# Optimization experiments

Hardware: AMD Instinct MI355X
Metric: run time of the kernel (lower is better)

The kernel has to match this reference:

```python
import jax, jax.numpy as jnp
import numpy as np

BLKQ = 64
BLKK = 64
TOPK_RATIO = 0.2


def setup_inputs() -> dict:
    key = jax.random.key(0)
    ks = jax.random.split(key, 5)
    B, H, L, D = 1, 16, 2048, 64
    q = jax.random.normal(ks[0], (B, H, L, D), dtype=jnp.float32)
    k = jax.random.normal(ks[1], (B, H, L, D), dtype=jnp.float32)
    v = jax.random.normal(ks[2], (B, H, L, D), dtype=jnp.float32)
    # proj_l params (zero-init in source; random here so the branch is exercised)
    W_proj = jax.random.normal(ks[3], (D, D), dtype=jnp.float32) * 0.02
    b_proj = jax.random.normal(ks[4], (D,), dtype=jnp.float32) * 0.02
    return {"q": q, "k": k, "v": v, "W_proj": W_proj, "b_proj": b_proj}


def _block_lut(q, k, topk_ratio, blkq, blkk):
    # q,k: [B,H,L,D]. Mean-pool blocks, score, take top-k key blocks per query block.
    B, H, L, D = q.shape
    M, N = L // blkq, L // blkk
    q_blocks = q.reshape(B, H, M, blkq, D).mean(axis=3)   # [B,H,M,D]
    k_blocks = k.reshape(B, H, N, blkk, D).mean(axis=3)   # [B,H,N,D]
    block_scores = jnp.einsum("bhmd,bhnd->bhmn", q_blocks, k_blocks)
    topk = min(N, max(1, int(topk_ratio * N)))
    _, lut = jax.lax.top_k(block_scores, topk)            # [B,H,M,topk] int32
    return lut, topk, M, N


def reference(q, k, v, W_proj, b_proj):
    B, H, L, D = q.shape
    lut, topk, M, N = _block_lut(q, k, TOPK_RATIO, BLKQ, BLKK)

    # ---- block-sparse softmax attention ----
    block_mask = jnp.any(jax.nn.one_hot(lut, N, dtype=jnp.bool_), axis=3)  # [B,H,M,N]
    mask = jnp.repeat(jnp.repeat(block_mask, BLKQ, axis=2), BLKK, axis=3)  # [B,H,L,L]
    scale = 1.0 / jnp.sqrt(jnp.asarray(D, q.dtype))
    scores = jnp.einsum("bhld,bhkd->bhlk", q, k) * scale
    scores = jnp.where(mask, scores, -jnp.inf)
    attn = jax.nn.softmax(scores, axis=-1)  # every row has >= topk*BLKK valid keys
    o_s = jnp.einsum("bhlk,bhkd->bhld", attn, v)

    # ---- linear attention (softmax feature map over D) ----
    q_feat = jax.nn.softmax(q, axis=-1)
    k_feat = jax.nn.softmax(k, axis=-1)
    kv_sum = jnp.einsum("bhld,bhle->bhde", k_feat, v)      # [B,H,D,D]
    k_sum = k_feat.sum(axis=2)                              # [B,H,D]
    num = jnp.einsum("bhld,bhde->bhle", q_feat, kv_sum)
    den = jnp.einsum("bhld,bhd->bhl", q_feat, k_sum)[..., None] + 1e-5
    o_l = num / den
    o_l = jnp.einsum("bhld,ed->bhle", o_l, W_proj) + b_proj  # nn.Linear: x @ W.T + b

    return o_s + o_l
```

## Files before the change

kernel.cpp:

```cpp
#include <hip/hip_runtime.h>
#include <math.h>

#define Hh 16
#define Ll 2048
#define Dd 64
#define MB 32
#define TK 6

typedef __attribute__((ext_vector_type(8))) short s16x8;
typedef __attribute__((ext_vector_type(4))) float f32x4;

static __device__ __forceinline__ unsigned short f2bf(float x) {
  unsigned int u = __float_as_uint(x);
  return (unsigned short)((u + 0x7fffu + ((u >> 16) & 1u)) >> 16);
}
static __device__ __forceinline__ float bf2f(short b) {
  return __uint_as_float(((unsigned int)(unsigned short)b) << 16);
}
static __device__ __forceinline__ int swz(int row, int bcol) {
  return row * 128 + (bcol ^ ((row & 7) << 4));
}

__global__ __launch_bounds__(256)
void k_prep(const float* __restrict__ q, const float* __restrict__ k,
            const float* __restrict__ v,
            unsigned short* __restrict__ qbf, unsigned short* __restrict__ kbf,
            unsigned short* __restrict__ vt,
            float* __restrict__ qb, float* __restrict__ kb,
            float* __restrict__ part_kv, float* __restrict__ part_ks) {
  __shared__ float tile[64][65];
  __shared__ float kf_s[64][68];
  __shared__ float v_sh[64][68];
  int hm = blockIdx.x;
  int h = hm >> 5, m = hm & 31;
  int t = threadIdx.x;
  int r = t >> 2, c0 = (t & 3) * 16;
  const size_t base = (size_t)hm * (64 * Dd);

  {
    float4 f[4];
#pragma unroll
    for (int i = 0; i < 4; ++i) {
      f[i] = *(const float4*)(q + base + r * Dd + c0 + i * 4);
      *(float4*)&tile[r][c0 + i * 4] = f[i];
      float4 vv = *(const float4*)(v + base + r * Dd + c0 + i * 4);
      *(float4*)&v_sh[r][c0 + i * 4] = vv;
    }
    const float* ff = (const float*)f;
    unsigned short* dst = qbf + base;
#pragma unroll
    for (int halfi = 0; halfi < 2; ++halfi) {
      s16x8 o;
#pragma unroll
      for (int j = 0; j < 8; ++j) o[j] = (short)f2bf(ff[halfi * 8 + j] * 0.125f);
      *(s16x8*)(dst + r * Dd + c0 + halfi * 8) = o;
    }
  }
  __syncthreads();
  if (t < 64) {
    float s = 0.f;
#pragma unroll 8
    for (int rr = 0; rr < 64; ++rr) s += tile[rr][t];
    qb[hm * 64 + t] = s * (1.0f / 64.0f);
  }
  {
    int d = t >> 2, kc = (t & 3) * 16;
    unsigned short* dst = vt + (size_t)h * Dd * Ll + (size_t)d * Ll + m * 64 + kc;
#pragma unroll
    for (int halfi = 0; halfi < 2; ++halfi) {
      s16x8 o;
#pragma unroll
      for (int j = 0; j < 8; ++j) o[j] = (short)f2bf(v_sh[kc + halfi * 8 + j][d]);
      *(s16x8*)(dst + halfi * 8) = o;
    }
  }
  __syncthreads();

  {
    float4 f[4];
#pragma unroll
    for (int i = 0; i < 4; ++i) {
      f[i] = *(const float4*)(k + base + r * Dd + c0 + i * 4);
      *(float4*)&tile[r][c0 + i * 4] = f[i];
    }
    const float* ff = (const float*)f;
    unsigned short* dst = kbf + base;
#pragma unroll
    for (int halfi = 0; halfi < 2; ++halfi) {
      s16x8 o;
#pragma unroll
      for (int j = 0; j < 8; ++j) o[j] = (short)f2bf(ff[halfi * 8 + j]);
      *(s16x8*)(dst + r * Dd + c0 + halfi * 8) = o;
    }
  }
  __syncthreads();
  if (t < 64) {
    float s = 0.f;
#pragma unroll 8
    for (int rr = 0; rr < 64; ++rr) s += tile[rr][t];
    kb[hm * 64 + t] = s * (1.0f / 64.0f);
  }
  {
    int rg = t >> 4;
    int c4 = (t & 15) * 4;
#pragma unroll
    for (int ch = 0; ch < 4; ++ch) {
      int rl = ch * 16 + rg;
      float4 kq = *(const float4*)&tile[rl][c4];
      float mx = fmaxf(fmaxf(kq.x, kq.y), fmaxf(kq.z, kq.w));
#pragma unroll
      for (int off = 8; off; off >>= 1) mx = fmaxf(mx, __shfl_xor(mx, off));
      float ex = __expf(kq.x - mx), ey = __expf(kq.y - mx);
      float ez = __expf(kq.z - mx), ew = __expf(kq.w - mx);
      float sm = ex + ey + ez + ew;
#pragma unroll
      for (int off = 8; off; off >>= 1) sm += __shfl_xor(sm, off);
      float inv = 1.0f / sm;
      *(float4*)&kf_s[rl][c4] = make_float4(ex * inv, ey * inv, ez * inv, ew * inv);
    }
  }
  __syncthreads();
  {
    int da0 = (t >> 4) * 4, e0 = (t & 15) * 4;
    float kvacc[4][4] = {};
    float ks4[4] = {0.f, 0.f, 0.f, 0.f};
    for (int rr = 0; rr < 64; ++rr) {
      float4 kf = *(const float4*)&kf_s[rr][da0];
      float4 vv = *(const float4*)&v_sh[rr][e0];
      ks4[0] += kf.x; ks4[1] += kf.y; ks4[2] += kf.z; ks4[3] += kf.w;
      kvacc[0][0] += kf.x * vv.x; kvacc[0][1] += kf.x * vv.y; kvacc[0][2] += kf.x * vv.z; kvacc[0][3] += kf.x * vv.w;
      kvacc[1][0] += kf.y * vv.x; kvacc[1][1] += kf.y * vv.y; kvacc[1][2] += kf.y * vv.z; kvacc[1][3] += kf.y * vv.w;
      kvacc[2][0] += kf.z * vv.x; kvacc[2][1] += kf.z * vv.y; kvacc[2][2] += kf.z * vv.z; kvacc[2][3] += kf.z * vv.w;
      kvacc[3][0] += kf.w * vv.x; kvacc[3][1] += kf.w * vv.y; kvacc[3][2] += kf.w * vv.z; kvacc[3][3] += kf.w * vv.w;
    }
    float* pkv = part_kv + (size_t)hm * 4096;
#pragma unroll
    for (int i = 0; i < 4; ++i)
      *(float4*)(pkv + (da0 + i) * 64 + e0) =
          make_float4(kvacc[i][0], kvacc[i][1], kvacc[i][2], kvacc[i][3]);
    if ((t & 15) == 0) {
#pragma unroll
      for (int i = 0; i < 4; ++i) part_ks[hm * 64 + da0 + i] = ks4[i];
    }
  }
}

__global__ __launch_bounds__(256)
void k_topk_fold(const float* __restrict__ qb, const float* __restrict__ kb,
                 int* __restrict__ lut,
                 const float* __restrict__ part_kv, const float* __restrict__ part_ks,
                 const float* __restrict__ W, float* __restrict__ ksum,
                 unsigned short* __restrict__ kvwt) {
  __shared__ float kvr[16][68];
  __shared__ float w_s[64][65];
  int blk = blockIdx.x;
  int t = threadIdx.x;
  if (blk < 128) {
    int w = t >> 6, l = t & 63;
    int hm = blk * 4 + w;
    int hh = hm >> 5;
    float val = -INFINITY;
    if (l < 32) {
      const float* qv = qb + hm * 64;
      const float* kv = kb + (hh * 32 + l) * 64;
      float s = 0.f;
#pragma unroll 8
      for (int d = 0; d < 64; ++d) s += qv[d] * kv[d];
      val = s;
    }
    int idx = l & 31;
    for (int t6 = 0; t6 < TK; ++t6) {
      float bv = val; int bi = idx;
#pragma unroll
      for (int off = 32; off; off >>= 1) {
        float ov = __shfl_xor(bv, off);
        int oi = __shfl_xor(bi, off);
        if (ov > bv || (ov == bv && oi < bi)) { bv = ov; bi = oi; }
      }
      if (l == 0) lut[hm * TK + t6] = bi;
      if (idx == bi && l < 32) val = -INFINITY;
    }
  } else {
    int fidx = blk - 128;
    int h = fidx >> 2, qtr = fidx & 3;
    int a0 = qtr * 16;
    {
      int a = t >> 4, b4 = (t & 15) * 4;
      float4 acc = make_float4(0.f, 0.f, 0.f, 0.f);
      for (int cc = 0; cc < 32; ++cc) {
        float4 p = *(const float4*)(part_kv + (size_t)(h * 32 + cc) * 4096 + (a0 + a) * 64 + b4);
        acc.x += p.x; acc.y += p.y; acc.z += p.z; acc.w += p.w;
      }
      *(float4*)&kvr[a][b4] = acc;
      int r = t >> 2, cq = (t & 3) * 16;
#pragma unroll
      for (int j = 0; j < 16; ++j) w_s[r][cq + j] = W[r * 64 + cq + j];
      if (qtr == 0 && t < 64) {
        float s = 0.f;
        for (int cc = 0; cc < 32; ++cc) s += part_ks[(h * 32 + cc) * 64 + t];
        ksum[h * 64 + t] = s;
      }
    }
    __syncthreads();
    int e = t & 63, ag = t >> 6;
    float acc4[4] = {0.f, 0.f, 0.f, 0.f};
    for (int b = 0; b < 64; ++b) {
      float wv = w_s[e][b];
#pragma unroll
      for (int i = 0; i < 4; ++i) acc4[i] += kvr[ag * 4 + i][b] * wv;
    }
#pragma unroll
    for (int i = 0; i < 4; ++i)
      kvwt[h * 4096 + e * 64 + a0 + ag * 4 + i] = f2bf(acc4[i]);
  }
}

__global__ __launch_bounds__(256, 2)
void k_attn(const unsigned short* __restrict__ qbf,
            const unsigned short* __restrict__ kbf,
            const unsigned short* __restrict__ vt,
            const int* __restrict__ lut,
            const unsigned short* __restrict__ kvwt,
            const float* __restrict__ ksum, const float* __restrict__ bproj,
            float* __restrict__ out) {
  __shared__ unsigned short k_s[2][4096];
  __shared__ unsigned short v_s[2][4096];
  __shared__ unsigned short p_s[4][1024];
  __shared__ unsigned short kvwt_s[4096];
  __shared__ float ks_s[64], b_s[64];
  __shared__ float den_s[4][16];

  int bid = blockIdx.x;
  int hm = (bid & 7) * 64 + (bid >> 3);
  int h = hm >> 5, m = hm & 31;
  int t = threadIdx.x, w = t >> 6, l = t & 63;
  int g = l >> 4, c16 = l & 15;

  int nbs[TK];
#pragma unroll
  for (int i = 0; i < TK; ++i) nbs[i] = lut[hm * TK + i];

  const unsigned short* qg = qbf + ((size_t)h * Ll + m * 64) * Dd;
  s16x8 aq[2];
#pragma unroll
  for (int kc = 0; kc < 2; ++kc)
    aq[kc] = *(const s16x8*)(qg + (w * 16 + c16) * Dd + kc * 32 + g * 8);

#pragma unroll
  for (int cc = 0; cc < 2; ++cc) {
    int idx = t + cc * 256;
    int row = idx >> 3, col8 = idx & 7;
    s16x8 val = *(const s16x8*)(kvwt + h * 4096 + row * 64 + col8 * 8);
    *(s16x8*)&kvwt_s[swz(row, col8 * 16) >> 1] = val;
  }
  if (t < 64) { ks_s[t] = ksum[h * 64 + t]; b_s[t] = bproj[t]; }

  const unsigned short* kh = kbf + (size_t)h * Ll * Dd;
  const unsigned short* vh = vt + (size_t)h * Dd * Ll;

  auto stage = [&](int buf, int nb) {
    const unsigned short* kb = kh + nb * 64 * Dd;
    const unsigned short* vb = vh + nb * 64;
#pragma unroll
    for (int i = 0; i < 2; ++i) {
      int c = i * 256 + t;
      int row = c >> 3, sub = c & 7;
      int scol = (sub ^ (row & 7)) * 8;
      __builtin_amdgcn_global_load_lds(
          (const __attribute__((address_space(1))) void*)(kb + row * Dd + scol),
          (__attribute__((address_space(3))) void*)&k_s[buf][c * 8], 16, 0, 0);
    }
#pragma unroll
    for (int i = 0; i < 2; ++i) {
      int c = i * 256 + t;
      int row = c >> 3, sub = c & 7;
      int scol = (sub ^ (row & 7)) * 8;
      __builtin_amdgcn_global_load_lds(
          (const __attribute__((address_space(1))) void*)(vb + (size_t)row * Ll + scol),
          (__attribute__((address_space(3))) void*)&v_s[buf][c * 8], 16, 0, 0);
    }
  };

  float mrow[4] = {-INFINITY, -INFINITY, -INFINITY, -INFINITY};
  float lrow[4] = {0.f, 0.f, 0.f, 0.f};
  f32x4 o[4] = {};

  stage(0, nbs[0]);
  __syncthreads();

  for (int kbi = 0; kbi < TK; ++kbi) {
    int buf = kbi & 1;
    if (kbi + 1 < TK) stage(buf ^ 1, nbs[kbi + 1]);

    f32x4 s[4];
#pragma unroll
    for (int nt = 0; nt < 4; ++nt) {
      s16x8 b0 = *(const s16x8*)&k_s[buf][swz(nt * 16 + c16, g * 16) >> 1];
      s16x8 b1 = *(const s16x8*)&k_s[buf][swz(nt * 16 + c16, 64 + g * 16) >> 1];
      f32x4 z = {0.f, 0.f, 0.f, 0.f};
      z = __builtin_amdgcn_mfma_f32_16x16x32_bf16(aq[0], b0, z, 0, 0, 0);
      s[nt] = __builtin_amdgcn_mfma_f32_16x16x32_bf16(aq[1], b1, z, 0, 0, 0);
    }

#pragma unroll
    for (int r = 0; r < 4; ++r) {
      float mx = fmaxf(fmaxf(s[0][r], s[1][r]), fmaxf(s[2][r], s[3][r]));
#pragma unroll
      for (int off = 8; off; off >>= 1) mx = fmaxf(mx, __shfl_xor(mx, off));
      float nm = fmaxf(mrow[r], mx);
      float rs = __expf(mrow[r] - nm);
      float sum = 0.f;
      int qrow = g * 4 + r;
#pragma unroll
      for (int nt = 0; nt < 4; ++nt) {
        float pv = __expf(s[nt][r] - nm);
        sum += pv;
        p_s[w][swz(qrow, (nt * 16 + c16) * 2) >> 1] = f2bf(pv);
      }
#pragma unroll
      for (int off = 8; off; off >>= 1) sum += __shfl_xor(sum, off);
      lrow[r] = lrow[r] * rs + sum;
      mrow[r] = nm;
      o[0][r] *= rs; o[1][r] *= rs; o[2][r] *= rs; o[3][r] *= rs;
    }

    asm volatile("s_waitcnt lgkmcnt(0)" ::: "memory");
    __builtin_amdgcn_sched_barrier(0);

    s16x8 ap0 = *(const s16x8*)&p_s[w][swz(c16, g * 16) >> 1];
    s16x8 ap1 = *(const s16x8*)&p_s[w][swz(c16, 64 + g * 16) >> 1];
#pragma unroll
    for (int nt = 0; nt < 4; ++nt) {
      s16x8 b0 = *(const s16x8*)&v_s[buf][swz(nt * 16 + c16, g * 16) >> 1];
      s16x8 b1 = *(const s16x8*)&v_s[buf][swz(nt * 16 + c16, 64 + g * 16) >> 1];
      o[nt] = __builtin_amdgcn_mfma_f32_16x16x32_bf16(ap0, b0, o[nt], 0, 0, 0);
      o[nt] = __builtin_amdgcn_mfma_f32_16x16x32_bf16(ap1, b1, o[nt], 0, 0, 0);
    }
    __syncthreads();
  }

  float qf0[8], qf1[8];
  float mx = -INFINITY;
#pragma unroll
  for (int j = 0; j < 8; ++j) {
    qf0[j] = bf2f(aq[0][j]) * 8.f;
    qf1[j] = bf2f(aq[1][j]) * 8.f;
    mx = fmaxf(mx, fmaxf(qf0[j], qf1[j]));
  }
  mx = fmaxf(mx, __shfl_xor(mx, 16));
  mx = fmaxf(mx, __shfl_xor(mx, 32));
  float sm = 0.f;
#pragma unroll
  for (int j = 0; j < 8; ++j) {
    qf0[j] = __expf(qf0[j] - mx);
    qf1[j] = __expf(qf1[j] - mx);
    sm += qf0[j] + qf1[j];
  }
  sm += __shfl_xor(sm, 16);
  sm += __shfl_xor(sm, 32);
  float qinv = 1.0f / sm;
  float dp = 0.f;
#pragma unroll
  for (int j = 0; j < 8; ++j) {
    qf0[j] *= qinv; qf1[j] *= qinv;
    dp += qf0[j] * ks_s[g * 8 + j] + qf1[j] * ks_s[32 + g * 8 + j];
  }
  dp += __shfl_xor(dp, 16);
  dp += __shfl_xor(dp, 32);
  if (g == 0) den_s[w][c16] = dp + 1e-5f;
  s16x8 pa0, pa1;
#pragma unroll
  for (int j = 0; j < 8; ++j) {
    pa0[j] = (short)f2bf(qf0[j]);
    pa1[j] = (short)f2bf(qf1[j]);
  }
  asm volatile("s_waitcnt lgkmcnt(0)" ::: "memory");
  __builtin_amdgcn_sched_barrier(0);

  f32x4 ol[4];
#pragma unroll
  for (int nt = 0; nt < 4; ++nt) {
    s16x8 b0 = *(const s16x8*)&kvwt_s[swz(nt * 16 + c16, g * 16) >> 1];
    s16x8 b1 = *(const s16x8*)&kvwt_s[swz(nt * 16 + c16, 64 + g * 16) >> 1];
    f32x4 z = {0.f, 0.f, 0.f, 0.f};
    z = __builtin_amdgcn_mfma_f32_16x16x32_bf16(pa0, b0, z, 0, 0, 0);
    ol[nt] = __builtin_amdgcn_mfma_f32_16x16x32_bf16(pa1, b1, z, 0, 0, 0);
  }

  float* ob = out + ((size_t)h * Ll + m * 64 + w * 16) * Dd;
#pragma unroll
  for (int r = 0; r < 4; ++r) {
    float inv_l = 1.0f / lrow[r];
    int qrow = g * 4 + r;
    float invd = 1.0f / den_s[w][qrow];
#pragma unroll
    for (int nt = 0; nt < 4; ++nt)
      ob[qrow * Dd + nt * 16 + c16] =
          o[nt][r] * inv_l + ol[nt][r] * invd + b_s[nt * 16 + c16];
  }
}

extern "C" void kernel_launch(void* const* d_in, const int* in_sizes, int n_in,
                              void* d_out, int out_size, void* d_ws, size_t ws_size,
                              hipStream_t stream) {
  const float* q = (const float*)d_in[0];
  const float* k = (const float*)d_in[1];
  const float* v = (const float*)d_in[2];
  const float* W = (const float*)d_in[3];
  const float* b = (const float*)d_in[4];
  float* out = (float*)d_out;

  char* wsb = (char*)d_ws;
  unsigned short* qbf = (unsigned short*)(wsb);
  unsigned short* kbf = (unsigned short*)(wsb + 4194304);
  unsigned short* vt  = (unsigned short*)(wsb + 8388608);
  float* qb      = (float*)(wsb + 12582912);
  float* kb      = (float*)(wsb + 12713984);
  int*   lut     = (int*)(wsb + 12845056);
  float* part_kv = (float*)(wsb + 12857344);
  float* part_ks = (float*)(wsb + 21245952);
  float* ksum    = (float*)(wsb + 21377024);
  unsigned short* kvwt = (unsigned short*)(wsb + 21381120);

  k_prep<<<512, 256, 0, stream>>>(q, k, v, qbf, kbf, vt, qb, kb, part_kv, part_ks);
  k_topk_fold<<<192, 256, 0, stream>>>(qb, kb, lut, part_kv, part_ks, W, ksum, kvwt);
  k_attn<<<512, 256, 0, stream>>>(qbf, kbf, vt, lut, kvwt, ksum, b, out);
}
```

Before: 42.50 us.

## Fuse top-k into prep via last-block counter, store partial KV in bf16, restructure attention barriers

Top-k block selection moves into the prep kernel. The last block finishing for each head, found with an atomic counter, computes the LUT, so the fold kernel only reduces the KV partials. The KV partials are stored in bf16, halving their traffic. The attention kernel issues the first K/V stage before loading Q and the linear-attention weights, replaces the trailing syncthreads with a waitcnt plus barrier at the top of the loop, and raises wave priority around the MFMA blocks. This adds an extra memset launch, serialises per-head top-k work onto one block, and accepts some bf16 rounding in the KV sums.

```diff
diff --git a/kernel.cpp b/kernel.cpp
--- a/kernel.cpp
+++ b/kernel.cpp
@@ -8,6 +8,7 @@
 #define TK 6
 
 typedef __attribute__((ext_vector_type(8))) short s16x8;
+typedef __attribute__((ext_vector_type(4))) short s16x4;
 typedef __attribute__((ext_vector_type(4))) float f32x4;
 
 static __device__ __forceinline__ unsigned short f2bf(float x) {
@@ -27,15 +28,18 @@
             unsigned short* __restrict__ qbf, unsigned short* __restrict__ kbf,
             unsigned short* __restrict__ vt,
             float* __restrict__ qb, float* __restrict__ kb,
-            float* __restrict__ part_kv, float* __restrict__ part_ks) {
+            unsigned short* __restrict__ part_kv, float* __restrict__ part_ks,
+            int* __restrict__ lut, int* __restrict__ cnt) {
   __shared__ float tile[64][65];
   __shared__ float kf_s[64][68];
   __shared__ float v_sh[64][68];
+  __shared__ int is_last;
   int hm = blockIdx.x;
-  int h = hm >> 5, m = hm & 31;
+  int h = hm >> 5;
   int t = threadIdx.x;
   int r = t >> 2, c0 = (t & 3) * 16;
   const size_t base = (size_t)hm * (64 * Dd);
+  int m = hm & 31;
 
   {
     float4 f[4];
@@ -133,86 +137,96 @@
       kvacc[2][0] += kf.z * vv.x; kvacc[2][1] += kf.z * vv.y; kvacc[2][2] += kf.z * vv.z; kvacc[2][3] += kf.z * vv.w;
       kvacc[3][0] += kf.w * vv.x; kvacc[3][1] += kf.w * vv.y; kvacc[3][2] += kf.w * vv.z; kvacc[3][3] += kf.w * vv.w;
     }
-    float* pkv = part_kv + (size_t)hm * 4096;
-#pragma unroll
-    for (int i = 0; i < 4; ++i)
-      *(float4*)(pkv + (da0 + i) * 64 + e0) =
-          make_float4(kvacc[i][0], kvacc[i][1], kvacc[i][2], kvacc[i][3]);
+    unsigned short* pkv = part_kv + (size_t)hm * 4096;
+#pragma unroll
+    for (int i = 0; i < 4; ++i) {
+      s16x4 o;
+      o[0] = (short)f2bf(kvacc[i][0]); o[1] = (short)f2bf(kvacc[i][1]);
+      o[2] = (short)f2bf(kvacc[i][2]); o[3] = (short)f2bf(kvacc[i][3]);
+      *(s16x4*)(pkv + (da0 + i) * 64 + e0) = o;
+    }
     if ((t & 15) == 0) {
 #pragma unroll
       for (int i = 0; i < 4; ++i) part_ks[hm * 64 + da0 + i] = ks4[i];
     }
   }
+
+  __threadfence();
+  __syncthreads();
+  if (t == 0) is_last = (atomicAdd(&cnt[h], 1) == 31) ? 1 : 0;
+  __syncthreads();
+  if (is_last) {
+    __threadfence();
+    int w = t >> 6, l = t & 63;
+    for (int qi = 0; qi < 8; ++qi) {
+      int hm2 = h * 32 + w * 8 + qi;
+      float val = -INFINITY;
+      if (l < 32) {
+        const float* qv = qb + hm2 * 64;
+        const float* kv = kb + (h * 32 + l) * 64;
+        float s = 0.f;
+#pragma unroll
+        for (int d4 = 0; d4 < 16; ++d4) {
+          float4 a = *(const float4*)(qv + d4 * 4);
+          float4 bb = *(const float4*)(kv + d4 * 4);
+          s += a.x * bb.x + a.y * bb.y + a.z * bb.z + a.w * bb.w;
+        }
+        val = s;
+      }
+      int idx = l & 31;
+      for (int t6 = 0; t6 < TK; ++t6) {
+        float bv = val; int bi = idx;
+#pragma unroll
+        for (int off = 32; off; off >>= 1) {
+          float ov = __shfl_xor(bv, off);
+          int oi = __shfl_xor(bi, off);
+          if (ov > bv || (ov == bv && oi < bi)) { bv = ov; bi = oi; }
+        }
+        if (l == 0) lut[hm2 * TK + t6] = bi;
+        if (idx == bi && l < 32) val = -INFINITY;
+      }
+    }
+  }
 }
 
 __global__ __launch_bounds__(256)
-void k_topk_fold(const float* __restrict__ qb, const float* __restrict__ kb,
-                 int* __restrict__ lut,
-                 const float* __restrict__ part_kv, const float* __restrict__ part_ks,
-                 const float* __restrict__ W, float* __restrict__ ksum,
-                 unsigned short* __restrict__ kvwt) {
+void k_fold(const unsigned short* __restrict__ part_kv, const float* __restrict__ part_ks,
+            const float* __restrict__ W, float* __restrict__ ksum,
+            unsigned short* __restrict__ kvwt) {
   __shared__ float kvr[16][68];
   __shared__ float w_s[64][65];
-  int blk = blockIdx.x;
+  int h = blockIdx.x >> 2, qtr = blockIdx.x & 3;
+  int a0 = qtr * 16;
   int t = threadIdx.x;
-  if (blk < 128) {
-    int w = t >> 6, l = t & 63;
-    int hm = blk * 4 + w;
-    int hh = hm >> 5;
-    float val = -INFINITY;
-    if (l < 32) {
-      const float* qv = qb + hm * 64;
-      const float* kv = kb + (hh * 32 + l) * 64;
+  {
+    int a = t >> 4, b4 = (t & 15) * 4;
+    float4 acc = make_float4(0.f, 0.f, 0.f, 0.f);
+    for (int cc = 0; cc < 32; ++cc) {
+      s16x4 p = *(const s16x4*)(part_kv + (size_t)(h * 32 + cc) * 4096 + (a0 + a) * 64 + b4);
+      acc.x += bf2f(p[0]); acc.y += bf2f(p[1]);
+      acc.z += bf2f(p[2]); acc.w += bf2f(p[3]);
+    }
+    *(float4*)&kvr[a][b4] = acc;
+    int r = t >> 2, cq = (t & 3) * 16;
+#pragma unroll
+    for (int j = 0; j < 16; ++j) w_s[r][cq + j] = W[r * 64 + cq + j];
+    if (qtr == 0 && t < 64) {
       float s = 0.f;
-#pragma unroll 8
-      for (int d = 0; d < 64; ++d) s += qv[d] * kv[d];
-      val = s;
-    }
-    int idx = l & 31;
-    for (int t6 = 0; t6 < TK; ++t6) {
-      float bv = val; int bi = idx;
-#pragma unroll
-      for (int off = 32; off; off >>= 1) {
-        float ov = __shfl_xor(bv, off);
-        int oi = __shfl_xor(bi, off);
-        if (ov > bv || (ov == bv && oi < bi)) { bv = ov; bi = oi; }
-      }
-      if (l == 0) lut[hm * TK + t6] = bi;
-      if (idx == bi && l < 32) val = -INFINITY;
-    }
-  } else {
-    int fidx = blk - 128;
-    int h = fidx >> 2, qtr = fidx & 3;
-    int a0 = qtr * 16;
-    {
-      int a = t >> 4, b4 = (t & 15) * 4;
-      float4 acc = make_float4(0.f, 0.f, 0.f, 0.f);
-      for (int cc = 0; cc < 32; ++cc) {
-        float4 p = *(const float4*)(part_kv + (size_t)(h * 32 + cc) * 4096 + (a0 + a) * 64 + b4);
-        acc.x += p.x; acc.y += p.y; acc.z += p.z; acc.w += p.w;
-      }
-      *(float4*)&kvr[a][b4] = acc;
-      int r = t >> 2, cq = (t & 3) * 16;
-#pragma unroll
-      for (int j = 0; j < 16; ++j) w_s[r][cq + j] = W[r * 64 + cq + j];
-      if (qtr == 0 && t < 64) {
-        float s = 0.f;
-        for (int cc = 0; cc < 32; ++cc) s += part_ks[(h * 32 + cc) * 64 + t];
-        ksum[h * 64 + t] = s;
-      }
-    }
-    __syncthreads();
-    int e = t & 63, ag = t >> 6;
-    float acc4[4] = {0.f, 0.f, 0.f, 0.f};
-    for (int b = 0; b < 64; ++b) {
-      float wv = w_s[e][b];
-#pragma unroll
-      for (int i = 0; i < 4; ++i) acc4[i] += kvr[ag * 4 + i][b] * wv;
-    }
-#pragma unroll
-    for (int i = 0; i < 4; ++i)
-      kvwt[h * 4096 + e * 64 + a0 + ag * 4 + i] = f2bf(acc4[i]);
-  }
+      for (int cc = 0; cc < 32; ++cc) s += part_ks[(h * 32 + cc) * 64 + t];
+      ksum[h * 64 + t] = s;
+    }
+  }
+  __syncthreads();
+  int e = t & 63, ag = t >> 6;
+  float acc4[4] = {0.f, 0.f, 0.f, 0.f};
+  for (int b = 0; b < 64; ++b) {
+    float wv = w_s[e][b];
+#pragma unroll
+    for (int i = 0; i < 4; ++i) acc4[i] += kvr[ag * 4 + i][b] * wv;
+  }
+#pragma unroll
+  for (int i = 0; i < 4; ++i)
+    kvwt[h * 4096 + e * 64 + a0 + ag * 4 + i] = f2bf(acc4[i]);
 }
 
 __global__ __launch_bounds__(256, 2)
@@ -240,21 +254,6 @@
 #pragma unroll
   for (int i = 0; i < TK; ++i) nbs[i] = lut[hm * TK + i];
 
-  const unsigned short* qg = qbf + ((size_t)h * Ll + m * 64) * Dd;
-  s16x8 aq[2];
-#pragma unroll
-  for (int kc = 0; kc < 2; ++kc)
-    aq[kc] = *(const s16x8*)(qg + (w * 16 + c16) * Dd + kc * 32 + g * 8);
-
-#pragma unroll
-  for (int cc = 0; cc < 2; ++cc) {
-    int idx = t + cc * 256;
-    int row = idx >> 3, col8 = idx & 7;
-    s16x8 val = *(const s16x8*)(kvwt + h * 4096 + row * 64 + col8 * 8);
-    *(s16x8*)&kvwt_s[swz(row, col8 * 16) >> 1] = val;
-  }
-  if (t < 64) { ks_s[t] = ksum[h * 64 + t]; b_s[t] = bproj[t]; }
-
   const unsigned short* kh = kbf + (size_t)h * Ll * Dd;
   const unsigned short* vh = vt + (size_t)h * Dd * Ll;
 
@@ -281,18 +280,37 @@
     }
   };
 
+  stage(0, nbs[0]);
+
+  const unsigned short* qg = qbf + ((size_t)h * Ll + m * 64) * Dd;
+  s16x8 aq[2];
+#pragma unroll
+  for (int kc = 0; kc < 2; ++kc)
+    aq[kc] = *(const s16x8*)(qg + (w * 16 + c16) * Dd + kc * 32 + g * 8);
+
+#pragma unroll
+  for (int cc = 0; cc < 2; ++cc) {
+    int idx = t + cc * 256;
+    int row = idx >> 3, col8 = idx & 7;
+    s16x8 val = *(const s16x8*)(kvwt + h * 4096 + row * 64 + col8 * 8);
+    *(s16x8*)&kvwt_s[swz(row, col8 * 16) >> 1] = val;
+  }
+  if (t < 64) { ks_s[t] = ksum[h * 64 + t]; b_s[t] = bproj[t]; }
+
   float mrow[4] = {-INFINITY, -INFINITY, -INFINITY, -INFINITY};
   float lrow[4] = {0.f, 0.f, 0.f, 0.f};
   f32x4 o[4] = {};
 
-  stage(0, nbs[0]);
-  __syncthreads();
-
   for (int kbi = 0; kbi < TK; ++kbi) {
     int buf = kbi & 1;
+    asm volatile("s_waitcnt vmcnt(0)" ::: "memory");
+    __builtin_amdgcn_sched_barrier(0);
+    __builtin_amdgcn_s_barrier();
+    __builtin_amdgcn_sched_barrier(0);
     if (kbi + 1 < TK) stage(buf ^ 1, nbs[kbi + 1]);
 
     f32x4 s[4];
+    __builtin_amdgcn_s_setprio(1);
 #pragma unroll
     for (int nt = 0; nt < 4; ++nt) {
       s16x8 b0 = *(const s16x8*)&k_s[buf][swz(nt * 16 + c16, g * 16) >> 1];
@@ -301,6 +319,7 @@
       z = __builtin_amdgcn_mfma_f32_16x16x32_bf16(aq[0], b0, z, 0, 0, 0);
       s[nt] = __builtin_amdgcn_mfma_f32_16x16x32_bf16(aq[1], b1, z, 0, 0, 0);
     }
+    __builtin_amdgcn_s_setprio(0);
 
 #pragma unroll
     for (int r = 0; r < 4; ++r) {
@@ -329,6 +348,7 @@
 
     s16x8 ap0 = *(const s16x8*)&p_s[w][swz(c16, g * 16) >> 1];
     s16x8 ap1 = *(const s16x8*)&p_s[w][swz(c16, 64 + g * 16) >> 1];
+    __builtin_amdgcn_s_setprio(1);
 #pragma unroll
     for (int nt = 0; nt < 4; ++nt) {
       s16x8 b0 = *(const s16x8*)&v_s[buf][swz(nt * 16 + c16, g * 16) >> 1];
@@ -336,7 +356,7 @@
       o[nt] = __builtin_amdgcn_mfma_f32_16x16x32_bf16(ap0, b0, o[nt], 0, 0, 0);
       o[nt] = __builtin_amdgcn_mfma_f32_16x16x32_bf16(ap1, b1, o[nt], 0, 0, 0);
     }
-    __syncthreads();
+    __builtin_amdgcn_s_setprio(0);
   }
 
   float qf0[8], qf1[8];
@@ -378,6 +398,7 @@
   __builtin_amdgcn_sched_barrier(0);
 
   f32x4 ol[4];
+  __builtin_amdgcn_s_setprio(1);
 #pragma unroll
   for (int nt = 0; nt < 4; ++nt) {
     s16x8 b0 = *(const s16x8*)&kvwt_s[swz(nt * 16 + c16, g * 16) >> 1];
@@ -386,6 +407,7 @@
     z = __builtin_amdgcn_mfma_f32_16x16x32_bf16(pa0, b0, z, 0, 0, 0);
     ol[nt] = __builtin_amdgcn_mfma_f32_16x16x32_bf16(pa1, b1, z, 0, 0, 0);
   }
+  __builtin_amdgcn_s_setprio(0);
 
   float* ob = out + ((size_t)h * Ll + m * 64 + w * 16) * Dd;
 #pragma unroll
@@ -417,12 +439,16 @@
   float* qb      = (float*)(wsb + 12582912);
   float* kb      = (float*)(wsb + 12713984);
   int*   lut     = (int*)(wsb + 12845056);
-  float* part_kv = (float*)(wsb + 12857344);
-  float* part_ks = (float*)(wsb + 21245952);
-  float* ksum    = (float*)(wsb + 21377024);
-  unsigned short* kvwt = (unsigned short*)(wsb + 21381120);
-
-  k_prep<<<512, 256, 0, stream>>>(q, k, v, qbf, kbf, vt, qb, kb, part_kv, part_ks);
-  k_topk_fold<<<192, 256, 0, stream>>>(qb, kb, lut, part_kv, part_ks, W, ksum, kvwt);
+  unsigned short* part_kv = (unsigned short*)(wsb + 12857344);
+  float* part_ks = (float*)(wsb + 17051648);
+  float* ksum    = (float*)(wsb + 17182720);
+  unsigned short* kvwt = (unsigned short*)(wsb + 17186816);
+  int*   cnt     = (int*)(wsb + 17317888);
+
+  hipMemsetAsync(cnt, 0, 64, stream);
+
+  k_prep<<<512, 256, 0, stream>>>(q, k, v, qbf, kbf, vt, qb, kb,
+                                  part_kv, part_ks, lut, cnt);
+  k_fold<<<64, 256, 0, stream>>>(part_kv, part_ks, W, ksum, kvwt);
   k_attn<<<512, 256, 0, stream>>>(qbf, kbf, vt, lut, kvwt, ksum, b, out);
 }
```

Result: slower. 145.5 us (+242.3%).
